# Kernel optimization log

Measured on AMD Instinct MI355X. Metric: run time of the kernel, lower is better.

## Reference

```python
import jax, jax.numpy as jnp
import numpy as np

B, T, F, H = 256, 128, 128, 512

def setup_inputs() -> dict:
    key = jax.random.key(0)
    ks = jax.random.split(key, 20)
    def xavier(k, shape):
        fan_in, fan_out = shape[1], shape[0]
        lim = np.sqrt(6.0 / (fan_in + fan_out)).astype(np.float32)
        return jax.random.uniform(k, shape, jnp.float32, -lim, lim)
    inp = {
        "x": jax.random.normal(ks[0], (B, T, F), jnp.float32),
        "m": (jax.random.uniform(ks[1], (B, T, F)) < 0.8).astype(jnp.float32),
        "d": jax.random.uniform(ks[2], (B, T, F), jnp.float32),
        "target_x": jax.random.normal(ks[3], (B, T, F), jnp.float32),
        "target_mask": (jax.random.uniform(ks[4], (B, T, F)) < 0.2).astype(jnp.float32),
        # TemporalDecay h: W [H,F], b [H]
        "td_h_W": xavier(ks[5], (H, F)), "td_h_b": jnp.zeros((H,), jnp.float32),
        # TemporalDecay x (diag): W [F,F], b [F]
        "td_x_W": xavier(ks[6], (F, F)), "td_x_b": jnp.zeros((F,), jnp.float32),
        # hist_reg Linear(H->F)
        "hist_W": xavier(ks[7], (F, H)), "hist_b": jnp.zeros((F,), jnp.float32),
        "feat_W": xavier(ks[8], (F, F)), "feat_b": jnp.zeros((F,), jnp.float32),
        # weight_combine Linear(2F->F)
        "wc_W": xavier(ks[9], (F, 2 * F)), "wc_b": jnp.zeros((F,), jnp.float32),
        # LSTMCell(2F -> H), PyTorch gate order i,f,g,o
        "W_ih": xavier(ks[10], (4 * H, 2 * F)), "W_hh": xavier(ks[11], (4 * H, H)),
        "b_ih": jnp.zeros((4 * H,), jnp.float32), "b_hh": jnp.zeros((4 * H,), jnp.float32),
    }
    return inp

def _rits_forward(x, m, d, target_x, target_mask,
                  td_h_W, td_h_b, td_x_W, td_x_b,
                  hist_W, hist_b, feat_W, feat_b, wc_W, wc_b,
                  W_ih, W_hh, b_ih, b_hh):
    Bx, Tx, Fx = x.shape
    Hx = td_h_W.shape[0]
    feat_mask = (1.0 - jnp.eye(Fx, dtype=x.dtype))
    feat_Wm_T = (feat_W * feat_mask).T              # [F,F]
    td_x_diag = jnp.diagonal(td_x_W)                # diag mask reduces matmul to elementwise

    def step(carry, inp):
        h, c, loss = carry
        x_t, m_t, d_t, tgt_t, ev_t = inp
        gamma_h = jnp.exp(-jax.nn.relu(d_t @ td_h_W.T + td_h_b))    # [B,H]
        gamma_x = jnp.exp(-jax.nn.relu(d_t * td_x_diag + td_x_b))   # [B,F]
        h = h * gamma_h
        x_hist = h @ hist_W.T + hist_b                              # [B,F]
        x_c = m_t * x_t + (1.0 - m_t) * x_hist
        z_h = x_c @ feat_Wm_T + feat_b
        alpha = jax.nn.sigmoid(jnp.concatenate([gamma_x, m_t], axis=1) @ wc_W.T + wc_b)
        c_h = alpha * z_h + (1.0 - alpha) * x_hist
        c_c = m_t * x_t + (1.0 - m_t) * c_h
        inputs = jnp.concatenate([c_c, m_t], axis=1)                # [B,2F]
        gates = inputs @ W_ih.T + b_ih + h @ W_hh.T + b_hh          # [B,4H]
        i_g, f_g, g_g, o_g = jnp.split(gates, 4, axis=1)
        c = jax.nn.sigmoid(f_g) * c + jax.nn.sigmoid(i_g) * jnp.tanh(g_g)
        h = jax.nn.sigmoid(o_g) * jnp.tanh(c)
        denom = ev_t.sum() + 1e-8
        loss = loss + (((x_hist - tgt_t) ** 2 * ev_t).sum()
                       + ((z_h - tgt_t) ** 2 * ev_t).sum()
                       + ((c_h - tgt_t) ** 2 * ev_t).sum()) / denom
        return (h, c, loss), c_c

    h0 = jnp.zeros((Bx, Hx), x.dtype)
    c0 = jnp.zeros((Bx, Hx), x.dtype)
    tm = lambda a: jnp.swapaxes(a, 0, 1)  # time-major [T,B,F]
    (_, _, loss), imps = jax.lax.scan(
        step, (h0, c0, jnp.float32(0.0)),
        (tm(x), tm(m), tm(d), tm(target_x), tm(target_mask)))
    imputations = jnp.swapaxes(imps, 0, 1)  # [B,T,F]
    return imputations, loss / max(Tx, 1)

def reference(x, m, d, target_x, target_mask,
              td_h_W, td_h_b, td_x_W, td_x_b,
              hist_W, hist_b, feat_W, feat_b, wc_W, wc_b,
              W_ih, W_hh, b_ih, b_hh):
    return _rits_forward(x, m, d, target_x, target_mask,
                         td_h_W, td_h_b, td_x_W, td_x_b,
                         hist_W, hist_b, feat_W, feat_b, wc_W, wc_b,
                         W_ih, W_hh, b_ih, b_hh)
```

## Files before the change

### kernel.cpp

```cpp
#include <hip/hip_runtime.h>

#define DEVINL __device__ __forceinline__

namespace {
constexpr int B = 256, T = 128, F = 128, H = 512;
constexpr int NBLK = 256;
constexpr int NTHR = 1024;

constexpr size_t OFF_NUM    = 0;
constexpr size_t OFF_DEN    = 128;
constexpr size_t OFF_WQCC   = 256;
constexpr size_t OFF_WQH    = OFF_WQCC + 64 * 2048;
constexpr size_t OFF_FSCC   = OFF_WQH + 128 * 2048;
constexpr size_t OFF_FSCHG  = OFF_FSCC + 2048;
constexpr size_t OFF_HISTQ  = OFF_FSCHG + 2048;
constexpr size_t OFF_FSCH   = OFF_HISTQ + 128 * 128;
constexpr size_t OFF_TD2    = OFF_FSCH + 128;
constexpr size_t OFF_FEAT2  = OFF_TD2 + 64 * 512;
constexpr size_t OFF_WC2    = OFF_FEAT2 + 64 * 128;
constexpr size_t OFF_BSUM   = OFF_WC2 + 128 * 128;
constexpr size_t OFF_FDIAG  = OFF_BSUM + 2048;
constexpr size_t WS_WORDS   = OFF_FDIAG + 128;

constexpr float ACT_S  = 15.875f;
constexpr float DEQ_CC = 1.f / (127.f * 15.875f);
constexpr float DEQ_H  = 1.f / (127.f * 127.f);

constexpr int FH = 0, FX = 1, FD = 2, FA = 3, FS = 4, FL = 5;
}

typedef _Float16 h2_t __attribute__((ext_vector_type(2)));

DEVINL h2_t as_h2(unsigned u) { union { unsigned u; h2_t h; } c; c.u = u; return c.h; }
DEVINL unsigned pack2(float a, float b) {
  union { h2_t h; unsigned u; } c;
  c.h = h2_t{(_Float16)a, (_Float16)b};
  return c.u;
}
DEVINL unsigned pack4i(int a, int b, int c, int d) {
  return (a & 0xFF) | ((b & 0xFF) << 8) | ((c & 0xFF) << 16) | ((d & 0xFF) << 24);
}

#if defined(__has_builtin)
#if __has_builtin(__builtin_amdgcn_fdot2)
#define HAVE_FDOT2 1
#endif
#if __has_builtin(__builtin_amdgcn_sdot4)
#define HAVE_SDOT4 1
#endif
#endif
#ifdef HAVE_FDOT2
DEVINL float fdot2(h2_t a, h2_t b, float c) { return __builtin_amdgcn_fdot2(a, b, c, false); }
#else
DEVINL float fdot2(h2_t a, h2_t b, float c) {
  return fmaf((float)a.x, (float)b.x, fmaf((float)a.y, (float)b.y, c));
}
#endif
#ifdef HAVE_SDOT4
DEVINL int sdot4(int a, int b, int c) { return __builtin_amdgcn_sdot4(a, b, c, false); }
#else
DEVINL int sdot4(int a, int b, int c) {
  return c + ((a << 24) >> 24) * ((b << 24) >> 24)
           + ((a << 16) >> 24) * ((b << 16) >> 24)
           + ((a << 8) >> 24) * ((b << 8) >> 24)
           + (a >> 24) * (b >> 24);
}
#endif

DEVINL float fast_sig(float x)  { return 1.f / (1.f + __expf(-x)); }
DEVINL float fast_tanh(float x) { return 1.f - 2.f / (1.f + __expf(2.f * x)); }

DEVINL float wave_sum(float v) {
#pragma unroll
  for (int s = 32; s; s >>= 1) v += __shfl_down(v, s, 64);
  return v;
}
DEVINL float wave_max(float v) {
#pragma unroll
  for (int s = 32; s; s >>= 1) v = fmaxf(v, __shfl_down(v, s, 64));
  return v;
}

DEVINL void flag_add(unsigned* p) {
  __hip_atomic_fetch_add(p, 1u, __ATOMIC_RELEASE, __HIP_MEMORY_SCOPE_WORKGROUP);
}
DEVINL void spin_ge(const unsigned* p, unsigned tgt) {
  int guard = 0;
  while (__hip_atomic_load(p, __ATOMIC_ACQUIRE, __HIP_MEMORY_SCOPE_WORKGROUP) < tgt) {
    __builtin_amdgcn_s_sleep(1);
    if (++guard > (1 << 24)) break;
  }
}

__global__ void prep_f16(const float* __restrict__ td_h_W, const float* __restrict__ feat_W,
                         const float* __restrict__ wc_W, const float* __restrict__ b_ih,
                         const float* __restrict__ b_hh,
                         unsigned* __restrict__ wsu, float* __restrict__ wsf) {
  int idx = blockIdx.x * blockDim.x + threadIdx.x;
  if (idx < 32768) {
    const int u = idx >> 6, k2 = idx & 63;
    wsu[OFF_TD2 + idx] = pack2(td_h_W[u * 128 + 2 * k2], td_h_W[u * 128 + 2 * k2 + 1]);
  } else if (idx < 40960) {
    const int i = idx - 32768, f = i >> 6, k2 = i & 63;
    wsu[OFF_FEAT2 + i] = pack2(feat_W[f * 128 + 2 * k2], feat_W[f * 128 + 2 * k2 + 1]);
  } else if (idx < 57344) {
    const int i = idx - 40960, f = i >> 7, k2 = i & 127;
    wsu[OFF_WC2 + i] = pack2(wc_W[f * 256 + 2 * k2], wc_W[f * 256 + 2 * k2 + 1]);
  } else if (idx < 59392) {
    const int i = idx - 57344, unit = i >> 2, g = i & 3;
    wsf[OFF_BSUM + i] = b_ih[g * 512 + unit] + b_hh[g * 512 + unit];
  } else if (idx < 59520) {
    const int f = idx - 59392;
    wsf[OFF_FDIAG + f] = (float)(_Float16)feat_W[f * 129];
  }
}

__global__ void prep_quant_wih(const float* __restrict__ Wih,
                               unsigned* __restrict__ wq, float* __restrict__ fscc) {
  const int col = blockIdx.x;
  const int unit = col >> 2, g = col & 3;
  const float* src = Wih + (size_t)(g * 512 + unit) * 256;
  const int t = threadIdx.x;
  const float4 v = ((const float4*)src)[t];
  float mx = fmaxf(fmaxf(fabsf(v.x), fabsf(v.y)), fmaxf(fabsf(v.z), fabsf(v.w)));
  mx = wave_max(mx);
  mx = __shfl(mx, 0, 64);
  const float s = (mx > 0.f) ? 127.f / mx : 0.f;
  wq[t * 2048 + col] = pack4i(__float2int_rn(v.x * s), __float2int_rn(v.y * s),
                              __float2int_rn(v.z * s), __float2int_rn(v.w * s));
  if (t == 0) fscc[col] = mx * DEQ_CC;
}

__global__ void prep_quant_whh(const float* __restrict__ Whh,
                               unsigned* __restrict__ wq, float* __restrict__ fschg) {
  const int col = blockIdx.x;
  const int unit = col >> 2, g = col & 3;
  const float* src = Whh + (size_t)(g * 512 + unit) * 512;
  const int t = threadIdx.x;
  const float4 v = ((const float4*)src)[t];
  float mx = fmaxf(fmaxf(fabsf(v.x), fabsf(v.y)), fmaxf(fabsf(v.z), fabsf(v.w)));
  mx = wave_max(mx);
  __shared__ float wm[2];
  if ((t & 63) == 0) wm[t >> 6] = mx;
  __syncthreads();
  const float maxv = fmaxf(wm[0], wm[1]);
  const float s = (maxv > 0.f) ? 127.f / maxv : 0.f;
  wq[t * 2048 + col] = pack4i(__float2int_rn(v.x * s), __float2int_rn(v.y * s),
                              __float2int_rn(v.z * s), __float2int_rn(v.w * s));
  if (t == 0) fschg[col] = maxv * DEQ_H;
}

__global__ void prep_quant_hist(const float* __restrict__ histW,
                                unsigned* __restrict__ histq, float* __restrict__ fsch) {
  const int f = blockIdx.x;
  const float* src = histW + (size_t)f * 512;
  const int t = threadIdx.x;
  const float4 v = ((const float4*)src)[t];
  float mx = fmaxf(fmaxf(fabsf(v.x), fabsf(v.y)), fmaxf(fabsf(v.z), fabsf(v.w)));
  mx = wave_max(mx);
  __shared__ float wm[2];
  if ((t & 63) == 0) wm[t >> 6] = mx;
  __syncthreads();
  const float maxv = fmaxf(wm[0], wm[1]);
  const float s = (maxv > 0.f) ? 127.f / maxv : 0.f;
  histq[f * 128 + t] = pack4i(__float2int_rn(v.x * s), __float2int_rn(v.y * s),
                              __float2int_rn(v.z * s), __float2int_rn(v.w * s));
  if (t == 0) fsch[f] = maxv * DEQ_H;
}

__global__ void __launch_bounds__(NTHR) rits_batch(
    const float* __restrict__ x, const float* __restrict__ m, const float* __restrict__ d,
    const float* __restrict__ tx, const float* __restrict__ tmask,
    const float* __restrict__ td_h_b, const float* __restrict__ td_x_W,
    const float* __restrict__ td_x_b, const float* __restrict__ hist_b,
    const float* __restrict__ feat_b, const float* __restrict__ wc_b,
    const unsigned* __restrict__ wsu, const float* __restrict__ wsf,
    float* __restrict__ num, float* __restrict__ den, float* __restrict__ out)
{
  const int tid = threadIdx.x;
  const int row = blockIdx.x;

  __shared__ __align__(16) unsigned hq_s[128];
  __shared__ __align__(16) unsigned actq_s[2][64];
  __shared__ __align__(16) unsigned gxm2_s[2][128];
  __shared__ __align__(16) unsigned d2_s[64];
  __shared__ __align__(16) unsigned xc2_s[64];
  __shared__ __align__(16) float gexp_s[512];
  __shared__ __align__(16) float h_s[512];
  __shared__ __align__(16) int4 partH_s[4][512];
  __shared__ __align__(16) int4 partC_s[2][512];
  __shared__ unsigned flg[6];

  if (tid < 512) { h_s[tid] = 0.f; gexp_s[tid] = 0.f; }
  if (tid < 6) flg[tid] = 0u;
  __syncthreads();

  if (tid < 128) {
    const int f = tid;
    const float hb = hist_b[f], fb = feat_b[f], wb = wc_b[f];
    const float fd = wsf[OFF_FDIAG + f], fsf = wsf[OFF_FSCH + f];
    const float dxw = td_x_W[f * 129], dxb = td_x_b[f];
    const float4 tdb4 = *(const float4*)(td_h_b + 4 * tid);

    float x_r, m_r, d_r, tx_r, ev_r;
    {
      const size_t b0 = (size_t)row * T * F + f;
      x_r = x[b0]; m_r = m[b0]; d_r = d[b0]; tx_r = tx[b0]; ev_r = tmask[b0];
      const float gx = __expf(-fmaxf(fmaf(d_r, dxw, dxb), 0.f));
      const float gxs = __shfl_down(gx, 1, 64);
      const float ms  = __shfl_down(m_r, 1, 64);
      if (!(f & 1)) {
        gxm2_s[0][f >> 1] = pack2(gx, gxs);
        gxm2_s[0][64 + (f >> 1)] = pack2(m_r, ms);
      }
      const int qm = __float2int_rn(m_r * ACT_S);
      const int q1 = __shfl_down(qm, 1, 64), q2 = __shfl_down(qm, 2, 64), q3 = __shfl_down(qm, 3, 64);
      if (!(f & 3)) actq_s[0][32 + (f >> 2)] = pack4i(qm, q1, q2, q3);
    }

    for (int t = 0; t < T; ++t) {
      const size_t base = ((size_t)row * T + t) * F;
      const int par = t & 1;

      if (t) { spin_ge(&flg[FL], 8u * (unsigned)t); __threadfence_block(); }
      {
        const float4 h4 = *(const float4*)(h_s + 4 * tid);
        const float4 g4 = *(const float4*)(gexp_s + 4 * tid);
        hq_s[tid] = pack4i(__float2int_rn(h4.x * g4.x * 127.f),
                           __float2int_rn(h4.y * g4.y * 127.f),
                           __float2int_rn(h4.z * g4.z * 127.f),
                           __float2int_rn(h4.w * g4.w * 127.f));
      }
      __threadfence_block();
      if (!(tid & 63)) flag_add(&flg[FH]);
      spin_ge(&flg[FH], 2u * (unsigned)(t + 1)); __threadfence_block();

      int is = 0;
      {
        const uint4* hw = (const uint4*)(wsu + OFF_HISTQ + (size_t)f * 128);
        const uint4* hq4 = (const uint4*)hq_s;
#pragma unroll 8
        for (int k = 0; k < 32; ++k) {
          const uint4 w = hw[k], a = hq4[k];
          is = sdot4((int)w.x, (int)a.x, is);
          is = sdot4((int)w.y, (int)a.y, is);
          is = sdot4((int)w.z, (int)a.z, is);
          is = sdot4((int)w.w, (int)a.w, is);
        }
      }
      const float xh = fmaf((float)is, fsf, hb);
      const float xc = m_r * x_r + (1.f - m_r) * xh;
      {
        const float xcs = __shfl_down(xc, 1, 64);
        if (!(f & 1)) xc2_s[f >> 1] = pack2(xc, xcs);
      }
      __threadfence_block();
      if (!(tid & 63)) flag_add(&flg[FX]);
      spin_ge(&flg[FX], 2u * (unsigned)(t + 1)); __threadfence_block();

      float z = fb, aa = wb;
      {
        const uint4* fw = (const uint4*)(wsu + OFF_FEAT2 + (size_t)f * 64);
        const uint4* xw = (const uint4*)xc2_s;
#pragma unroll 8
        for (int k = 0; k < 16; ++k) {
          const uint4 w = fw[k], v = xw[k];
          z = fdot2(as_h2(w.x), as_h2(v.x), z);
          z = fdot2(as_h2(w.y), as_h2(v.y), z);
          z = fdot2(as_h2(w.z), as_h2(v.z), z);
          z = fdot2(as_h2(w.w), as_h2(v.w), z);
        }
        const uint4* ww = (const uint4*)(wsu + OFF_WC2 + (size_t)f * 128);
        const uint4* gw = (const uint4*)gxm2_s[par];
#pragma unroll 8
        for (int k = 0; k < 32; ++k) {
          const uint4 w = ww[k], g = gw[k];
          aa = fdot2(as_h2(w.x), as_h2(g.x), aa);
          aa = fdot2(as_h2(w.y), as_h2(g.y), aa);
          aa = fdot2(as_h2(w.z), as_h2(g.z), aa);
          aa = fdot2(as_h2(w.w), as_h2(g.w), aa);
        }
      }
      z -= xc * fd;
      const float al = fast_sig(aa);
      const float ch = al * z + (1.f - al) * xh;
      const float cc = m_r * x_r + (1.f - m_r) * ch;
      out[base + f] = cc;
      const float e1 = xh - tx_r, e2 = z - tx_r, e3 = ch - tx_r;
      const float s1 = wave_sum(ev_r * (e1 * e1 + e2 * e2 + e3 * e3));
      const float s2 = wave_sum(ev_r);
      if (!(tid & 63)) { atomicAdd(&num[t], s1); atomicAdd(&den[t], s2); }

      {
        const int qc = __float2int_rn(fminf(fmaxf(cc, -8.f), 8.f) * ACT_S);
        const int c1 = __shfl_down(qc, 1, 64), c2 = __shfl_down(qc, 2, 64), c3 = __shfl_down(qc, 3, 64);
        if (!(f & 3)) actq_s[par][f >> 2] = pack4i(qc, c1, c2, c3);
      }
      __threadfence_block();
      if (!(tid & 63)) flag_add(&flg[FA]);

      if (t + 1 < T) {
        const size_t b2 = base + F + f;
        x_r = x[b2]; m_r = m[b2]; d_r = d[b2]; tx_r = tx[b2]; ev_r = tmask[b2];
        const float gx = __expf(-fmaxf(fmaf(d_r, dxw, dxb), 0.f));
        const float gxs = __shfl_down(gx, 1, 64);
        const float ms  = __shfl_down(m_r, 1, 64);
        const float dsh = __shfl_down(d_r, 1, 64);
        if (!(f & 1)) {
          gxm2_s[par ^ 1][f >> 1] = pack2(gx, gxs);
          gxm2_s[par ^ 1][64 + (f >> 1)] = pack2(m_r, ms);
          d2_s[f >> 1] = pack2(d_r, dsh);
        }
        const int qm = __float2int_rn(m_r * ACT_S);
        const int q1 = __shfl_down(qm, 1, 64), q2 = __shfl_down(qm, 2, 64), q3 = __shfl_down(qm, 3, 64);
        if (!(f & 3)) actq_s[par ^ 1][32 + (f >> 2)] = pack4i(qm, q1, q2, q3);
        __threadfence_block();
        if (!(tid & 63)) flag_add(&flg[FD]);
        spin_ge(&flg[FD], 2u * (unsigned)(t + 1)); __threadfence_block();
        float g0 = tdb4.x, g1 = tdb4.y, g2 = tdb4.z, g3 = tdb4.w;
        const uint4* t0 = (const uint4*)(wsu + OFF_TD2 + ((size_t)tid * 4) * 64);
        const uint4* dw = (const uint4*)d2_s;
#pragma unroll 4
        for (int k = 0; k < 16; ++k) {
          const uint4 dd = dw[k];
          uint4 w = t0[k];
          g0 = fdot2(as_h2(w.x), as_h2(dd.x), g0); g0 = fdot2(as_h2(w.y), as_h2(dd.y), g0);
          g0 = fdot2(as_h2(w.z), as_h2(dd.z), g0); g0 = fdot2(as_h2(w.w), as_h2(dd.w), g0);
          w = t0[k + 16];
          g1 = fdot2(as_h2(w.x), as_h2(dd.x), g1); g1 = fdot2(as_h2(w.y), as_h2(dd.y), g1);
          g1 = fdot2(as_h2(w.z), as_h2(dd.z), g1); g1 = fdot2(as_h2(w.w), as_h2(dd.w), g1);
          w = t0[k + 32];
          g2 = fdot2(as_h2(w.x), as_h2(dd.x), g2); g2 = fdot2(as_h2(w.y), as_h2(dd.y), g2);
          g2 = fdot2(as_h2(w.z), as_h2(dd.z), g2); g2 = fdot2(as_h2(w.w), as_h2(dd.w), g2);
          w = t0[k + 48];
          g3 = fdot2(as_h2(w.x), as_h2(dd.x), g3); g3 = fdot2(as_h2(w.y), as_h2(dd.y), g3);
          g3 = fdot2(as_h2(w.z), as_h2(dd.z), g3); g3 = fdot2(as_h2(w.w), as_h2(dd.w), g3);
        }
        *(float4*)(gexp_s + 4 * tid) = float4{
            __expf(-fmaxf(g0, 0.f)), __expf(-fmaxf(g1, 0.f)),
            __expf(-fmaxf(g2, 0.f)), __expf(-fmaxf(g3, 0.f))};
      }
    }
  } else {
    const int st = tid - 128;
    float4 bs{}, fscc4{}, fsch4{};
    float c0 = 0.f;
    if (st < 512) {
      bs    = *(const float4*)(wsf + OFF_BSUM  + 4 * st);
      fscc4 = *(const float4*)(wsf + OFF_FSCC  + 4 * st);
      fsch4 = *(const float4*)(wsf + OFF_FSCHG + 4 * st);
    }
    for (int t = 0; t < T; ++t) {
      const int par = t & 1;
      const unsigned tg = (unsigned)(t + 1);
      spin_ge(&flg[FH], 2u * tg); __threadfence_block();
#pragma unroll 1
      for (int it = 0; it < 4; ++it) {
        const int j = st + 896 * it;
        if (j >= 3072) break;
        if (j < 2048) {
          const int unit = j & 511, kq = j >> 9;
          const uint4* wp = (const uint4*)(wsu + OFF_WQH) + (size_t)(kq * 32) * 512 + unit;
          const unsigned* aw = hq_s + kq * 32;
          int4 acc{0, 0, 0, 0};
#pragma unroll 8
          for (int k = 0; k < 32; ++k) {
            const uint4 w = wp[(size_t)k * 512];
            const int a0 = (int)aw[k];
            acc.x = sdot4((int)w.x, a0, acc.x);
            acc.y = sdot4((int)w.y, a0, acc.y);
            acc.z = sdot4((int)w.z, a0, acc.z);
            acc.w = sdot4((int)w.w, a0, acc.w);
          }
          partH_s[kq][unit] = acc;
        } else {
          const int jj = j - 2048;
          const int unit = jj & 511;
          const int kh = 1 - (jj >> 9);
          if (kh == 0) { spin_ge(&flg[FA], 2u * tg); __threadfence_block(); }
          const uint4* wp = (const uint4*)(wsu + OFF_WQCC) + (size_t)(kh * 32) * 512 + unit;
          const unsigned* aw = actq_s[par] + kh * 32;
          int4 acc{0, 0, 0, 0};
#pragma unroll 8
          for (int k = 0; k < 32; ++k) {
            const uint4 w = wp[(size_t)k * 512];
            const int a0 = (int)aw[k];
            acc.x = sdot4((int)w.x, a0, acc.x);
            acc.y = sdot4((int)w.y, a0, acc.y);
            acc.z = sdot4((int)w.z, a0, acc.z);
            acc.w = sdot4((int)w.w, a0, acc.w);
          }
          partC_s[kh][unit] = acc;
        }
      }
      __threadfence_block();
      if (!(tid & 63)) flag_add(&flg[FS]);
      spin_ge(&flg[FS], 14u * tg); __threadfence_block();

      if (st < 512) {
        const int4 p0 = partH_s[0][st], p1 = partH_s[1][st],
                   p2 = partH_s[2][st], p3 = partH_s[3][st];
        const int4 q0 = partC_s[0][st], q1 = partC_s[1][st];
        const float ai = bs.x + fscc4.x * (float)(q0.x + q1.x) + fsch4.x * (float)(p0.x + p1.x + p2.x + p3.x);
        const float af = bs.y + fscc4.y * (float)(q0.y + q1.y) + fsch4.y * (float)(p0.y + p1.y + p2.y + p3.y);
        const float ag = bs.z + fscc4.z * (float)(q0.z + q1.z) + fsch4.z * (float)(p0.z + p1.z + p2.z + p3.z);
        const float ao = bs.w + fscc4.w * (float)(q0.w + q1.w) + fsch4.w * (float)(p0.w + p1.w + p2.w + p3.w);
        const float ig = fast_sig(ai), fg = fast_sig(af);
        const float gg = fast_tanh(ag), og = fast_sig(ao);
        c0 = fg * c0 + ig * gg;
        h_s[st] = og * fast_tanh(c0);
        __threadfence_block();
        if (!(tid & 63)) flag_add(&flg[FL]);
      }
    }
  }
}

__global__ void finalize(const float* __restrict__ num, const float* __restrict__ den,
                         float* __restrict__ out) {
  __shared__ float red[2];
  const int t = threadIdx.x;
  float v = num[t] / (den[t] + 1e-8f);
  v = wave_sum(v);
  if ((t & 63) == 0) red[t >> 6] = v;
  __syncthreads();
  if (t == 0) out[(size_t)B * T * F] = (red[0] + red[1]) / (float)T;
}

extern "C" void kernel_launch(void* const* d_in, const int* in_sizes, int n_in,
                              void* d_out, int out_size, void* d_ws, size_t ws_size,
                              hipStream_t stream) {
  const float* x      = (const float*)d_in[0];
  const float* m      = (const float*)d_in[1];
  const float* d      = (const float*)d_in[2];
  const float* tx     = (const float*)d_in[3];
  const float* tmask  = (const float*)d_in[4];
  const float* td_h_W = (const float*)d_in[5];
  const float* td_h_b = (const float*)d_in[6];
  const float* td_x_W = (const float*)d_in[7];
  const float* td_x_b = (const float*)d_in[8];
  const float* hist_W = (const float*)d_in[9];
  const float* hist_b = (const float*)d_in[10];
  const float* feat_W = (const float*)d_in[11];
  const float* feat_b = (const float*)d_in[12];
  const float* wc_W   = (const float*)d_in[13];
  const float* wc_b   = (const float*)d_in[14];
  const float* W_ih   = (const float*)d_in[15];
  const float* W_hh   = (const float*)d_in[16];
  const float* b_ih   = (const float*)d_in[17];
  const float* b_hh   = (const float*)d_in[18];

  float*    wsf = (float*)d_ws;
  unsigned* wsu = (unsigned*)d_ws;
  float*    out = (float*)d_out;

  if (ws_size < WS_WORDS * 4) return;

  hipMemsetAsync(d_ws, 0, 256 * sizeof(float), stream);
  prep_f16<<<dim3((59520 + 255) / 256), dim3(256), 0, stream>>>(
      td_h_W, feat_W, wc_W, b_ih, b_hh, wsu, wsf);
  prep_quant_wih<<<dim3(2048), dim3(64), 0, stream>>>(
      W_ih, wsu + OFF_WQCC, wsf + OFF_FSCC);
  prep_quant_whh<<<dim3(2048), dim3(128), 0, stream>>>(
      W_hh, wsu + OFF_WQH, wsf + OFF_FSCHG);
  prep_quant_hist<<<dim3(128), dim3(128), 0, stream>>>(
      hist_W, wsu + OFF_HISTQ, wsf + OFF_FSCH);
  rits_batch<<<dim3(NBLK), dim3(NTHR), 0, stream>>>(
      x, m, d, tx, tmask, td_h_b, td_x_W, td_x_b, hist_b, feat_b, wc_b,
      wsu, wsf, wsf + OFF_NUM, wsf + OFF_DEN, out);
  finalize<<<dim3(1), dim3(128), 0, stream>>>(wsf + OFF_NUM, wsf + OFF_DEN, out);
}
```

Before: 3.037 ms.

## Replace spin-flag warp specialization with barrier-phased schedule and distributed streaming jobs

Drops the producer/consumer flag-and-spin protocol between the 128 feature threads and 896 gate threads, and runs each timestep as a sequence of __syncthreads phases instead. The recurrent int8 gate matmuls and the temporal-decay gamma_h matvec are spread across the idle threads while the feature threads do the history and feature regressions. The cc-dependent gate part is computed by all 1024 threads once cc is ready. Next-step inputs are prefetched into shared memory by otherwise idle threads. The aim is to remove spin-wait latency and serialization of the gamma_h computation, at the cost of block-wide barriers that keep all waves in lockstep.

```diff
diff --git a/kernel.cpp b/kernel.cpp
--- a/kernel.cpp
+++ b/kernel.cpp
@@ -25,8 +25,6 @@
 constexpr float ACT_S  = 15.875f;
 constexpr float DEQ_CC = 1.f / (127.f * 15.875f);
 constexpr float DEQ_H  = 1.f / (127.f * 127.f);
-
-constexpr int FH = 0, FX = 1, FD = 2, FA = 3, FS = 4, FL = 5;
 }
 
 typedef _Float16 h2_t __attribute__((ext_vector_type(2)));
@@ -79,17 +77,6 @@
 #pragma unroll
   for (int s = 32; s; s >>= 1) v = fmaxf(v, __shfl_down(v, s, 64));
   return v;
-}
-
-DEVINL void flag_add(unsigned* p) {
-  __hip_atomic_fetch_add(p, 1u, __ATOMIC_RELEASE, __HIP_MEMORY_SCOPE_WORKGROUP);
-}
-DEVINL void spin_ge(const unsigned* p, unsigned tgt) {
-  int guard = 0;
-  while (__hip_atomic_load(p, __ATOMIC_ACQUIRE, __HIP_MEMORY_SCOPE_WORKGROUP) < tgt) {
-    __builtin_amdgcn_s_sleep(1);
-    if (++guard > (1 << 24)) break;
-  }
 }
 
 __global__ void prep_f16(const float* __restrict__ td_h_W, const float* __restrict__ feat_W,
@@ -168,6 +155,64 @@
   if (t == 0) fsch[f] = maxv * DEQ_H;
 }
 
+DEVINL void stream_job(int j, int parTD,
+                       const unsigned* __restrict__ wsu, const float* __restrict__ td_h_b,
+                       const unsigned* hq_s, const unsigned* actq_s, const unsigned* d2b_s,
+                       float* gexp_s, int4* partH_s, int4* partCm_s) {
+  if (j < 2048) {
+    const int unit = j & 511, q = j >> 9;
+    const unsigned* wp = wsu + OFF_WQH + 4 * unit + ((size_t)(32 * q) << 11);
+    const unsigned* aw = hq_s + 32 * q;
+    int4 acc{0, 0, 0, 0};
+#pragma unroll 8
+    for (int k = 0; k < 32; ++k) {
+      const uint4 w = *(const uint4*)(wp + ((size_t)k << 11));
+      const int a0 = (int)aw[k];
+      acc.x = sdot4((int)w.x, a0, acc.x);
+      acc.y = sdot4((int)w.y, a0, acc.y);
+      acc.z = sdot4((int)w.z, a0, acc.z);
+      acc.w = sdot4((int)w.w, a0, acc.w);
+    }
+    partH_s[q * 512 + unit] = acc;
+  } else if (j < 2560) {
+    const int unit = j - 2048;
+    const unsigned* wp = wsu + OFF_WQCC + 4 * unit + ((size_t)32 << 11);
+    const unsigned* aw = actq_s + 32;
+    int4 acc{0, 0, 0, 0};
+#pragma unroll 8
+    for (int k = 0; k < 32; ++k) {
+      const uint4 w = *(const uint4*)(wp + ((size_t)k << 11));
+      const int a0 = (int)aw[k];
+      acc.x = sdot4((int)w.x, a0, acc.x);
+      acc.y = sdot4((int)w.y, a0, acc.y);
+      acc.z = sdot4((int)w.z, a0, acc.z);
+      acc.w = sdot4((int)w.w, a0, acc.w);
+    }
+    partCm_s[unit] = acc;
+  } else {
+    const int up = j - 2560;
+    const uint4* t0 = (const uint4*)(wsu + OFF_TD2 + (size_t)(2 * up) * 64);
+    const uint4* dw = (const uint4*)(d2b_s + parTD * 64);
+    float g0 = td_h_b[2 * up], g1 = td_h_b[2 * up + 1];
+#pragma unroll 4
+    for (int k = 0; k < 16; ++k) {
+      const uint4 dd = dw[k];
+      uint4 w = t0[k];
+      g0 = fdot2(as_h2(w.x), as_h2(dd.x), g0);
+      g0 = fdot2(as_h2(w.y), as_h2(dd.y), g0);
+      g0 = fdot2(as_h2(w.z), as_h2(dd.z), g0);
+      g0 = fdot2(as_h2(w.w), as_h2(dd.w), g0);
+      w = t0[k + 16];
+      g1 = fdot2(as_h2(w.x), as_h2(dd.x), g1);
+      g1 = fdot2(as_h2(w.y), as_h2(dd.y), g1);
+      g1 = fdot2(as_h2(w.z), as_h2(dd.z), g1);
+      g1 = fdot2(as_h2(w.w), as_h2(dd.w), g1);
+    }
+    gexp_s[2 * up]     = __expf(-fmaxf(g0, 0.f));
+    gexp_s[2 * up + 1] = __expf(-fmaxf(g1, 0.f));
+  }
+}
+
 __global__ void __launch_bounds__(NTHR) rits_batch(
     const float* __restrict__ x, const float* __restrict__ m, const float* __restrict__ d,
     const float* __restrict__ tx, const float* __restrict__ tmask,
@@ -179,85 +224,99 @@
 {
   const int tid = threadIdx.x;
   const int row = blockIdx.x;
+  const int st = tid - 128;
 
   __shared__ __align__(16) unsigned hq_s[128];
-  __shared__ __align__(16) unsigned actq_s[2][64];
-  __shared__ __align__(16) unsigned gxm2_s[2][128];
-  __shared__ __align__(16) unsigned d2_s[64];
+  __shared__ __align__(16) unsigned actq_s[64];
   __shared__ __align__(16) unsigned xc2_s[64];
-  __shared__ __align__(16) float gexp_s[512];
-  __shared__ __align__(16) float h_s[512];
-  __shared__ __align__(16) int4 partH_s[4][512];
-  __shared__ __align__(16) int4 partC_s[2][512];
-  __shared__ unsigned flg[6];
-
-  if (tid < 512) { h_s[tid] = 0.f; gexp_s[tid] = 0.f; }
-  if (tid < 6) flg[tid] = 0u;
-  __syncthreads();
-
+  __shared__ __align__(16) unsigned gxm2_s[128];
+  __shared__ __align__(16) unsigned d2b_s[128];
+  __shared__ float x_s[128], m_s[128], tx_s[128], ev_s[128];
+  __shared__ float dxw_s[128], dxb_s[128];
+  __shared__ float gexp_s[512];
+  __shared__ __align__(16) int4 partH_s[4 * 512];
+  __shared__ __align__(16) int4 partCm_s[512];
+  __shared__ __align__(16) int4 partCc_s[2 * 512];
+
+  const int unit = tid & 511;
+  const float4 bs    = *(const float4*)(wsf + OFF_BSUM + 4 * unit);
+  const float4 fscc4 = *(const float4*)(wsf + OFF_FSCC + 4 * unit);
+  const float4 fsch4 = *(const float4*)(wsf + OFF_FSCHG + 4 * unit);
+  float hb = 0.f, fb = 0.f, wb = 0.f, fd = 0.f, fsf = 0.f;
   if (tid < 128) {
-    const int f = tid;
-    const float hb = hist_b[f], fb = feat_b[f], wb = wc_b[f];
-    const float fd = wsf[OFF_FDIAG + f], fsf = wsf[OFF_FSCH + f];
-    const float dxw = td_x_W[f * 129], dxb = td_x_b[f];
-    const float4 tdb4 = *(const float4*)(td_h_b + 4 * tid);
-
-    float x_r, m_r, d_r, tx_r, ev_r;
-    {
-      const size_t b0 = (size_t)row * T * F + f;
-      x_r = x[b0]; m_r = m[b0]; d_r = d[b0]; tx_r = tx[b0]; ev_r = tmask[b0];
-      const float gx = __expf(-fmaxf(fmaf(d_r, dxw, dxb), 0.f));
-      const float gxs = __shfl_down(gx, 1, 64);
-      const float ms  = __shfl_down(m_r, 1, 64);
-      if (!(f & 1)) {
-        gxm2_s[0][f >> 1] = pack2(gx, gxs);
-        gxm2_s[0][64 + (f >> 1)] = pack2(m_r, ms);
+    hb = hist_b[tid]; fb = feat_b[tid]; wb = wc_b[tid];
+    fd = wsf[OFF_FDIAG + tid]; fsf = wsf[OFF_FSCH + tid];
+  }
+
+  float h0 = 0.f, c0 = 0.f;
+
+  {
+    const size_t b0 = (size_t)row * T * F;
+    if (tid < 128) {
+      dxw_s[tid] = td_x_W[tid * 129];
+      dxb_s[tid] = td_x_b[tid];
+      hq_s[tid] = 0u;
+    } else if (tid < 160) {
+      const int w = tid - 128;
+      const size_t b4 = b0 + 4 * w;
+      actq_s[32 + w] = pack4i(__float2int_rn(m[b4] * ACT_S), __float2int_rn(m[b4 + 1] * ACT_S),
+                              __float2int_rn(m[b4 + 2] * ACT_S), __float2int_rn(m[b4 + 3] * ACT_S));
+    } else if (tid < 224) {
+      const int j = tid - 160;
+      d2b_s[64 + j] = pack2(d[b0 + F + 2 * j], d[b0 + F + 2 * j + 1]);
+    } else if (tid >= 512) {
+      const int s3 = tid - 512, a = s3 >> 7, f2 = s3 & 127;
+      const float v = (a == 0 ? x[b0 + f2] : a == 1 ? m[b0 + f2]
+                       : a == 2 ? tx[b0 + f2] : tmask[b0 + f2]);
+      if      (a == 0) x_s[f2]  = v;
+      else if (a == 1) m_s[f2]  = v;
+      else if (a == 2) tx_s[f2] = v;
+      else             ev_s[f2] = v;
+    }
+    __syncthreads();
+    if (tid < 64) {
+      const float dv0 = d[b0 + 2 * tid], dv1 = d[b0 + 2 * tid + 1];
+      const float g0 = __expf(-fmaxf(fmaf(dv0, dxw_s[2 * tid], dxb_s[2 * tid]), 0.f));
+      const float g1 = __expf(-fmaxf(fmaf(dv1, dxw_s[2 * tid + 1], dxb_s[2 * tid + 1]), 0.f));
+      gxm2_s[tid] = pack2(g0, g1);
+    } else if (tid < 128) {
+      const int j = tid - 64;
+      gxm2_s[64 + j] = pack2(m[b0 + 2 * j], m[b0 + 2 * j + 1]);
+    }
+    __syncthreads();
+  }
+
+  for (int t = 0; t < T; ++t) {
+    const size_t base = ((size_t)row * T + t) * F;
+    const int parTD = (t + 1) & 1;
+    float xh = 0.f, xc = 0.f;
+
+    if (tid < 128) {
+      const int f = tid;
+      int is = 0;
+      const uint4* hw = (const uint4*)(wsu + OFF_HISTQ + (size_t)f * 128);
+      const uint4* hq4 = (const uint4*)hq_s;
+#pragma unroll 8
+      for (int k = 0; k < 32; ++k) {
+        const uint4 w = hw[k], a = hq4[k];
+        is = sdot4((int)w.x, (int)a.x, is);
+        is = sdot4((int)w.y, (int)a.y, is);
+        is = sdot4((int)w.z, (int)a.z, is);
+        is = sdot4((int)w.w, (int)a.w, is);
       }
-      const int qm = __float2int_rn(m_r * ACT_S);
-      const int q1 = __shfl_down(qm, 1, 64), q2 = __shfl_down(qm, 2, 64), q3 = __shfl_down(qm, 3, 64);
-      if (!(f & 3)) actq_s[0][32 + (f >> 2)] = pack4i(qm, q1, q2, q3);
-    }
-
-    for (int t = 0; t < T; ++t) {
-      const size_t base = ((size_t)row * T + t) * F;
-      const int par = t & 1;
-
-      if (t) { spin_ge(&flg[FL], 8u * (unsigned)t); __threadfence_block(); }
-      {
-        const float4 h4 = *(const float4*)(h_s + 4 * tid);
-        const float4 g4 = *(const float4*)(gexp_s + 4 * tid);
-        hq_s[tid] = pack4i(__float2int_rn(h4.x * g4.x * 127.f),
-                           __float2int_rn(h4.y * g4.y * 127.f),
-                           __float2int_rn(h4.z * g4.z * 127.f),
-                           __float2int_rn(h4.w * g4.w * 127.f));
-      }
-      __threadfence_block();
-      if (!(tid & 63)) flag_add(&flg[FH]);
-      spin_ge(&flg[FH], 2u * (unsigned)(t + 1)); __threadfence_block();
-
-      int is = 0;
-      {
-        const uint4* hw = (const uint4*)(wsu + OFF_HISTQ + (size_t)f * 128);
-        const uint4* hq4 = (const uint4*)hq_s;
-#pragma unroll 8
-        for (int k = 0; k < 32; ++k) {
-          const uint4 w = hw[k], a = hq4[k];
-          is = sdot4((int)w.x, (int)a.x, is);
-          is = sdot4((int)w.y, (int)a.y, is);
-          is = sdot4((int)w.z, (int)a.z, is);
-          is = sdot4((int)w.w, (int)a.w, is);
-        }
-      }
-      const float xh = fmaf((float)is, fsf, hb);
-      const float xc = m_r * x_r + (1.f - m_r) * xh;
-      {
-        const float xcs = __shfl_down(xc, 1, 64);
-        if (!(f & 1)) xc2_s[f >> 1] = pack2(xc, xcs);
-      }
-      __threadfence_block();
-      if (!(tid & 63)) flag_add(&flg[FX]);
-      spin_ge(&flg[FX], 2u * (unsigned)(t + 1)); __threadfence_block();
-
+      xh = fmaf((float)is, fsf, hb);
+      const float mv = m_s[f], xv = x_s[f];
+      xc = mv * xv + (1.f - mv) * xh;
+      const float xcs = __shfl_down(xc, 1, 64);
+      if (!(f & 1)) xc2_s[f >> 1] = pack2(xc, xcs);
+    } else if (t < T - 1) {
+      stream_job(st, parTD, wsu, td_h_b, hq_s, actq_s, d2b_s, gexp_s, partH_s, partCm_s);
+      stream_job(st + 896, parTD, wsu, td_h_b, hq_s, actq_s, d2b_s, gexp_s, partH_s, partCm_s);
+    }
+    __syncthreads();
+
+    if (tid < 128) {
+      const int f = tid;
       float z = fb, aa = wb;
       {
         const uint4* fw = (const uint4*)(wsu + OFF_FEAT2 + (size_t)f * 64);
@@ -271,7 +330,7 @@
           z = fdot2(as_h2(w.w), as_h2(v.w), z);
         }
         const uint4* ww = (const uint4*)(wsu + OFF_WC2 + (size_t)f * 128);
-        const uint4* gw = (const uint4*)gxm2_s[par];
+        const uint4* gw = (const uint4*)gxm2_s;
 #pragma unroll 8
         for (int k = 0; k < 32; ++k) {
           const uint4 w = ww[k], g = gw[k];
@@ -284,135 +343,97 @@
       z -= xc * fd;
       const float al = fast_sig(aa);
       const float ch = al * z + (1.f - al) * xh;
-      const float cc = m_r * x_r + (1.f - m_r) * ch;
+      const float mv = m_s[f], xv = x_s[f];
+      const float cc = mv * xv + (1.f - mv) * ch;
       out[base + f] = cc;
-      const float e1 = xh - tx_r, e2 = z - tx_r, e3 = ch - tx_r;
-      const float s1 = wave_sum(ev_r * (e1 * e1 + e2 * e2 + e3 * e3));
-      const float s2 = wave_sum(ev_r);
+      const float tg = tx_s[f], evv = ev_s[f];
+      const float e1 = xh - tg, e2 = z - tg, e3 = ch - tg;
+      const float s1 = wave_sum(evv * (e1 * e1 + e2 * e2 + e3 * e3));
+      const float s2 = wave_sum(evv);
       if (!(tid & 63)) { atomicAdd(&num[t], s1); atomicAdd(&den[t], s2); }
-
-      {
-        const int qc = __float2int_rn(fminf(fmaxf(cc, -8.f), 8.f) * ACT_S);
-        const int c1 = __shfl_down(qc, 1, 64), c2 = __shfl_down(qc, 2, 64), c3 = __shfl_down(qc, 3, 64);
-        if (!(f & 3)) actq_s[par][f >> 2] = pack4i(qc, c1, c2, c3);
+      const int qc = __float2int_rn(fminf(fmaxf(cc, -8.f), 8.f) * ACT_S);
+      const int c1 = __shfl_down(qc, 1, 64), c2 = __shfl_down(qc, 2, 64), c3 = __shfl_down(qc, 3, 64);
+      if (!(f & 3)) actq_s[f >> 2] = pack4i(qc, c1, c2, c3);
+    } else if (t < T - 1) {
+      stream_job(1792 + st, parTD, wsu, td_h_b, hq_s, actq_s, d2b_s, gexp_s, partH_s, partCm_s);
+      if (st < 128)
+        stream_job(2688 + st, parTD, wsu, td_h_b, hq_s, actq_s, d2b_s, gexp_s, partH_s, partCm_s);
+    }
+    __syncthreads();
+
+    if (t == T - 1) break;
+
+    {
+      const int kh = tid >> 9;
+      const unsigned* wp = wsu + OFF_WQCC + 4 * unit + ((size_t)(kh * 16) << 11);
+      const unsigned* aw = actq_s + kh * 16;
+      int4 acc{0, 0, 0, 0};
+#pragma unroll 8
+      for (int k = 0; k < 16; ++k) {
+        const uint4 w = *(const uint4*)(wp + ((size_t)k << 11));
+        const int a0 = (int)aw[k];
+        acc.x = sdot4((int)w.x, a0, acc.x);
+        acc.y = sdot4((int)w.y, a0, acc.y);
+        acc.z = sdot4((int)w.z, a0, acc.z);
+        acc.w = sdot4((int)w.w, a0, acc.w);
       }
-      __threadfence_block();
-      if (!(tid & 63)) flag_add(&flg[FA]);
-
-      if (t + 1 < T) {
-        const size_t b2 = base + F + f;
-        x_r = x[b2]; m_r = m[b2]; d_r = d[b2]; tx_r = tx[b2]; ev_r = tmask[b2];
-        const float gx = __expf(-fmaxf(fmaf(d_r, dxw, dxb), 0.f));
-        const float gxs = __shfl_down(gx, 1, 64);
-        const float ms  = __shfl_down(m_r, 1, 64);
-        const float dsh = __shfl_down(d_r, 1, 64);
-        if (!(f & 1)) {
-          gxm2_s[par ^ 1][f >> 1] = pack2(gx, gxs);
-          gxm2_s[par ^ 1][64 + (f >> 1)] = pack2(m_r, ms);
-          d2_s[f >> 1] = pack2(d_r, dsh);
-        }
-        const int qm = __float2int_rn(m_r * ACT_S);
-        const int q1 = __shfl_down(qm, 1, 64), q2 = __shfl_down(qm, 2, 64), q3 = __shfl_down(qm, 3, 64);
-        if (!(f & 3)) actq_s[par ^ 1][32 + (f >> 2)] = pack4i(qm, q1, q2, q3);
-        __threadfence_block();
-        if (!(tid & 63)) flag_add(&flg[FD]);
-        spin_ge(&flg[FD], 2u * (unsigned)(t + 1)); __threadfence_block();
-        float g0 = tdb4.x, g1 = tdb4.y, g2 = tdb4.z, g3 = tdb4.w;
-        const uint4* t0 = (const uint4*)(wsu + OFF_TD2 + ((size_t)tid * 4) * 64);
-        const uint4* dw = (const uint4*)d2_s;
-#pragma unroll 4
-        for (int k = 0; k < 16; ++k) {
-          const uint4 dd = dw[k];
-          uint4 w = t0[k];
-          g0 = fdot2(as_h2(w.x), as_h2(dd.x), g0); g0 = fdot2(as_h2(w.y), as_h2(dd.y), g0);
-          g0 = fdot2(as_h2(w.z), as_h2(dd.z), g0); g0 = fdot2(as_h2(w.w), as_h2(dd.w), g0);
-          w = t0[k + 16];
-          g1 = fdot2(as_h2(w.x), as_h2(dd.x), g1); g1 = fdot2(as_h2(w.y), as_h2(dd.y), g1);
-          g1 = fdot2(as_h2(w.z), as_h2(dd.z), g1); g1 = fdot2(as_h2(w.w), as_h2(dd.w), g1);
-          w = t0[k + 32];
-          g2 = fdot2(as_h2(w.x), as_h2(dd.x), g2); g2 = fdot2(as_h2(w.y), as_h2(dd.y), g2);
-          g2 = fdot2(as_h2(w.z), as_h2(dd.z), g2); g2 = fdot2(as_h2(w.w), as_h2(dd.w), g2);
-          w = t0[k + 48];
-          g3 = fdot2(as_h2(w.x), as_h2(dd.x), g3); g3 = fdot2(as_h2(w.y), as_h2(dd.y), g3);
-          g3 = fdot2(as_h2(w.z), as_h2(dd.z), g3); g3 = fdot2(as_h2(w.w), as_h2(dd.w), g3);
-        }
-        *(float4*)(gexp_s + 4 * tid) = float4{
-            __expf(-fmaxf(g0, 0.f)), __expf(-fmaxf(g1, 0.f)),
-            __expf(-fmaxf(g2, 0.f)), __expf(-fmaxf(g3, 0.f))};
-      }
-    }
-  } else {
-    const int st = tid - 128;
-    float4 bs{}, fscc4{}, fsch4{};
-    float c0 = 0.f;
-    if (st < 512) {
-      bs    = *(const float4*)(wsf + OFF_BSUM  + 4 * st);
-      fscc4 = *(const float4*)(wsf + OFF_FSCC  + 4 * st);
-      fsch4 = *(const float4*)(wsf + OFF_FSCHG + 4 * st);
-    }
-    for (int t = 0; t < T; ++t) {
-      const int par = t & 1;
-      const unsigned tg = (unsigned)(t + 1);
-      spin_ge(&flg[FH], 2u * tg); __threadfence_block();
-#pragma unroll 1
-      for (int it = 0; it < 4; ++it) {
-        const int j = st + 896 * it;
-        if (j >= 3072) break;
-        if (j < 2048) {
-          const int unit = j & 511, kq = j >> 9;
-          const uint4* wp = (const uint4*)(wsu + OFF_WQH) + (size_t)(kq * 32) * 512 + unit;
-          const unsigned* aw = hq_s + kq * 32;
-          int4 acc{0, 0, 0, 0};
-#pragma unroll 8
-          for (int k = 0; k < 32; ++k) {
-            const uint4 w = wp[(size_t)k * 512];
-            const int a0 = (int)aw[k];
-            acc.x = sdot4((int)w.x, a0, acc.x);
-            acc.y = sdot4((int)w.y, a0, acc.y);
-            acc.z = sdot4((int)w.z, a0, acc.z);
-            acc.w = sdot4((int)w.w, a0, acc.w);
-          }
-          partH_s[kq][unit] = acc;
-        } else {
-          const int jj = j - 2048;
-          const int unit = jj & 511;
-          const int kh = 1 - (jj >> 9);
-          if (kh == 0) { spin_ge(&flg[FA], 2u * tg); __threadfence_block(); }
-          const uint4* wp = (const uint4*)(wsu + OFF_WQCC) + (size_t)(kh * 32) * 512 + unit;
-          const unsigned* aw = actq_s[par] + kh * 32;
-          int4 acc{0, 0, 0, 0};
-#pragma unroll 8
-          for (int k = 0; k < 32; ++k) {
-            const uint4 w = wp[(size_t)k * 512];
-            const int a0 = (int)aw[k];
-            acc.x = sdot4((int)w.x, a0, acc.x);
-            acc.y = sdot4((int)w.y, a0, acc.y);
-            acc.z = sdot4((int)w.z, a0, acc.z);
-            acc.w = sdot4((int)w.w, a0, acc.w);
-          }
-          partC_s[kh][unit] = acc;
+      partCc_s[kh * 512 + unit] = acc;
+    }
+    __syncthreads();
+
+    if (tid < 512) {
+      const int4 p0 = partH_s[unit], p1 = partH_s[512 + unit];
+      const int4 p2 = partH_s[1024 + unit], p3 = partH_s[1536 + unit];
+      const int4 cm = partCm_s[unit];
+      const int4 q0 = partCc_s[unit], q1 = partCc_s[512 + unit];
+      const float ai = bs.x + fscc4.x * (float)(cm.x + q0.x + q1.x)
+                     + fsch4.x * (float)(p0.x + p1.x + p2.x + p3.x);
+      const float af = bs.y + fscc4.y * (float)(cm.y + q0.y + q1.y)
+                     + fsch4.y * (float)(p0.y + p1.y + p2.y + p3.y);
+      const float ag = bs.z + fscc4.z * (float)(cm.z + q0.z + q1.z)
+                     + fsch4.z * (float)(p0.z + p1.z + p2.z + p3.z);
+      const float ao = bs.w + fscc4.w * (float)(cm.w + q0.w + q1.w)
+                     + fsch4.w * (float)(p0.w + p1.w + p2.w + p3.w);
+      const float ig = fast_sig(ai), fg = fast_sig(af);
+      const float gg = fast_tanh(ag), og = fast_sig(ao);
+      c0 = fg * c0 + ig * gg;
+      h0 = og * fast_tanh(c0);
+      const float hv = h0 * gexp_s[tid];
+      int q = __float2int_rn(hv * 127.f);
+      const int a1 = __shfl_down(q, 1, 64), a2 = __shfl_down(q, 2, 64), a3 = __shfl_down(q, 3, 64);
+      if (!(tid & 3)) hq_s[tid >> 2] = pack4i(q, a1, a2, a3);
+      const size_t b1 = base + F;
+      if (tid < 64) {
+        const float dv0 = d[b1 + 2 * tid], dv1 = d[b1 + 2 * tid + 1];
+        const float g0 = __expf(-fmaxf(fmaf(dv0, dxw_s[2 * tid], dxb_s[2 * tid]), 0.f));
+        const float g1 = __expf(-fmaxf(fmaf(dv1, dxw_s[2 * tid + 1], dxb_s[2 * tid + 1]), 0.f));
+        gxm2_s[tid] = pack2(g0, g1);
+      } else if (tid < 128) {
+        const int j = tid - 64;
+        gxm2_s[64 + j] = pack2(m[b1 + 2 * j], m[b1 + 2 * j + 1]);
+      } else if (tid < 160) {
+        const int w = tid - 128;
+        const size_t b4 = b1 + 4 * w;
+        actq_s[32 + w] = pack4i(__float2int_rn(m[b4] * ACT_S), __float2int_rn(m[b4 + 1] * ACT_S),
+                                __float2int_rn(m[b4 + 2] * ACT_S), __float2int_rn(m[b4 + 3] * ACT_S));
+      } else if (tid < 224) {
+        if (t + 2 < T) {
+          const int j = tid - 160;
+          const size_t b2 = base + 2 * F;
+          d2b_s[((t + 2) & 1) * 64 + j] = pack2(d[b2 + 2 * j], d[b2 + 2 * j + 1]);
         }
       }
-      __threadfence_block();
-      if (!(tid & 63)) flag_add(&flg[FS]);
-      spin_ge(&flg[FS], 14u * tg); __threadfence_block();
-
-      if (st < 512) {
-        const int4 p0 = partH_s[0][st], p1 = partH_s[1][st],
-                   p2 = partH_s[2][st], p3 = partH_s[3][st];
-        const int4 q0 = partC_s[0][st], q1 = partC_s[1][st];
-        const float ai = bs.x + fscc4.x * (float)(q0.x + q1.x) + fsch4.x * (float)(p0.x + p1.x + p2.x + p3.x);
-        const float af = bs.y + fscc4.y * (float)(q0.y + q1.y) + fsch4.y * (float)(p0.y + p1.y + p2.y + p3.y);
-        const float ag = bs.z + fscc4.z * (float)(q0.z + q1.z) + fsch4.z * (float)(p0.z + p1.z + p2.z + p3.z);
-        const float ao = bs.w + fscc4.w * (float)(q0.w + q1.w) + fsch4.w * (float)(p0.w + p1.w + p2.w + p3.w);
-        const float ig = fast_sig(ai), fg = fast_sig(af);
-        const float gg = fast_tanh(ag), og = fast_sig(ao);
-        c0 = fg * c0 + ig * gg;
-        h_s[st] = og * fast_tanh(c0);
-        __threadfence_block();
-        if (!(tid & 63)) flag_add(&flg[FL]);
-      }
-    }
+    } else {
+      const int s3 = tid - 512, a = s3 >> 7, f2 = s3 & 127;
+      const size_t b1 = base + F;
+      const float v = (a == 0 ? x[b1 + f2] : a == 1 ? m[b1 + f2]
+                       : a == 2 ? tx[b1 + f2] : tmask[b1 + f2]);
+      if      (a == 0) x_s[f2]  = v;
+      else if (a == 1) m_s[f2]  = v;
+      else if (a == 2) tx_s[f2] = v;
+      else             ev_s[f2] = v;
+    }
+    __syncthreads();
   }
 }
 
```

After: 3.814 ms. 25.6% more time.
